# Performance work log

Measured on AMD Instinct MI355X. Metric: run time of the kernel, lower is better.

## Reference

```python
import jax, jax.numpy as jnp
import numpy as np

D_MODEL = 1024
NUM_HEADS = 16
OUT_SHAPE = (64,)            # ControlGate `shape`; d_head = prod(OUT_SHAPE)
BANK_SIZE = 16
TOP_K = 2
BATCH, SEQ = 8, 4096
D_OUT = NUM_HEADS * int(np.prod(OUT_SHAPE))  # 1024


def setup_inputs() -> dict:
    key = jax.random.key(0)
    k1, k2, k3, k4 = jax.random.split(key, 4)
    tensor = jax.random.normal(k1, (BATCH, SEQ, D_MODEL), dtype=jnp.float32)
    sel_idx = jax.random.randint(k2, (BATCH, TOP_K), 0, BANK_SIZE)
    sel_probs = jax.random.uniform(k3, (BATCH, TOP_K), dtype=jnp.float32)
    sel_probs = sel_probs / jnp.sum(sel_probs, axis=-1, keepdims=True)
    W = jax.random.normal(k4, (BANK_SIZE, D_MODEL, D_OUT), dtype=jnp.float32) * 0.02
    b = jnp.zeros((BANK_SIZE, D_OUT), dtype=jnp.float32)
    return {"tensor": tensor, "sel_idx": sel_idx, "sel_probs": sel_probs, "W": W, "b": b}


def reference(tensor, sel_idx, sel_probs, W, b):
    # --- VirtualMakeHeads: bank-selected (virtual) linear projection ---
    # Superimpose the selected weight banks per batch element.
    W_sel = W[sel_idx]                    # (B, K, d_model, d_out)  irregular gather
    b_sel = b[sel_idx]                    # (B, K, d_out)
    W_eff = jnp.einsum('bk,bkio->bio', sel_probs, W_sel)   # (B, d_model, d_out)
    b_eff = jnp.einsum('bk,bko->bo', sel_probs, b_sel)     # (B, d_out)
    logits = jnp.einsum('bsi,bio->bso', tensor, W_eff) + b_eff[:, None, :]
    # reshape to heads: (B, S, num_heads, d_head)
    logits = logits.reshape(*logits.shape[:-1], NUM_HEADS, -1)
    # --- ControlGate: unflatten last dim into OUT_SHAPE ---
    logits = logits.reshape(*logits.shape[:-1], *OUT_SHAPE)
    # DropoutLogits with p=0.0 (eval) is identity.
    # activation == 'sigmoid'
    return jax.nn.sigmoid(logits)
```

## Files before the change

### kernel.cpp

```cpp
#include <hip/hip_runtime.h>
#include <hip/hip_bf16.h>

#define B_  8
#define S_  4096
#define DM  1024
#define DO  1024

typedef __attribute__((ext_vector_type(4))) float f32x4;
typedef __attribute__((ext_vector_type(8))) short bf16x8;

__device__ inline unsigned int pkbf(float a, float b) {
    __hip_bfloat162 h = __float22bfloat162_rn(float2{a, b});
    union { __hip_bfloat162 h2; unsigned int u; } cv;
    cv.h2 = h;
    return cv.u;
}

__global__ __launch_bounds__(256) void prep_wpack(
    const float* __restrict__ W, const int* __restrict__ sel_idx,
    const float* __restrict__ sel_probs, unsigned short* __restrict__ wpack)
{
    const int kt = blockIdx.x, nb = blockIdx.y, b = blockIdx.z;
    const int i0 = sel_idx[b*2+0], i1 = sel_idx[b*2+1];
    const float p0 = sel_probs[b*2+0], p1 = sel_probs[b*2+1];
    const int col = threadIdx.x;
    const int half = col >> 7, colh = col & 127;

    const float* w0 = W + (size_t)i0 * DM * DO + (size_t)(kt * 64) * DO + nb * 256 + col;
    const float* w1 = W + (size_t)i1 * DM * DO + (size_t)(kt * 64) * DO + nb * 256 + col;

    char* dst = (char*)wpack + ((((size_t)b * 4 + nb) * 16 + kt) << 15)
              + half * 16384 + colh * 128;

    #pragma unroll
    for (int g = 0; g < 8; ++g) {
        float v[8];
        #pragma unroll
        for (int j = 0; j < 8; ++j)
            v[j] = p0 * w0[(size_t)(g * 8 + j) * DO] + p1 * w1[(size_t)(g * 8 + j) * DO];
        uint4 u;
        u.x = pkbf(v[0], v[1]); u.y = pkbf(v[2], v[3]);
        u.z = pkbf(v[4], v[5]); u.w = pkbf(v[6], v[7]);
        *reinterpret_cast<uint4*>(dst + ((g * 16) ^ ((colh & 7) << 4))) = u;
    }
}

__global__ __launch_bounds__(256) void prep_beff(
    const float* __restrict__ bias, const int* __restrict__ sel_idx,
    const float* __restrict__ sel_probs, float* __restrict__ beff)
{
    const int b = blockIdx.x;
    const int i0 = sel_idx[b*2+0], i1 = sel_idx[b*2+1];
    const float p0 = sel_probs[b*2+0], p1 = sel_probs[b*2+1];
    for (int o = threadIdx.x; o < DO; o += blockDim.x)
        beff[(size_t)b * DO + o] = p0 * bias[(size_t)i0 * DO + o]
                                 + p1 * bias[(size_t)i1 * DO + o];
}

__global__ __launch_bounds__(512, 1) void gemm8(
    const float* __restrict__ X, const unsigned short* __restrict__ wpack,
    const float* __restrict__ beff, float* __restrict__ out)
{
    extern __shared__ char lds[];

    const int id = blockIdx.x;
    const int swz = (id & 7) * 64 + (id >> 3);
    const int b  = swz >> 6;
    const int bm = (swz & 63) >> 2;
    const int nb = swz & 3;

    const int t = threadIdx.x;
    const int wave = t >> 6, lane = t & 63;
    const int wm = wave >> 2, wn = wave & 3;
    const int fr = lane & 15, fq = lane >> 4;

    const int s_row = t >> 3;
    const int s_g   = t & 7;
    const float* xbase = X + ((size_t)(b * S_ + bm * 256 + s_row)) * DM + s_g * 8;
    const char* wtile0 = (const char*)(wpack + (((size_t)b * 4 + nb) * 16) * 16384);

    const int swz0 = (fq * 16) ^ ((fr & 7) << 4);
    const int swz1 = (64 + fq * 16) ^ ((fr & 7) << 4);
    const int aTb = wm * 16384 + fr * 128;
    const int bTb = (wn >> 1) * 16384 + ((wn & 1) * 64 + fr) * 128;

    f32x4 acc[8][4] = {};
    float4 ax[8];

#define LOAD_X(KT)                                                            \
    _Pragma("unroll")                                                         \
    for (int p = 0; p < 4; ++p) {                                             \
        ax[p*2]   = *reinterpret_cast<const float4*>(xbase + (size_t)p*64*DM + (KT)*64);     \
        ax[p*2+1] = *reinterpret_cast<const float4*>(xbase + (size_t)p*64*DM + (KT)*64 + 4); \
    }

#define STAGE_B(KT, BOFF)                                                     \
    {                                                                         \
        const char* gB = wtile0 + (size_t)(KT) * 32768;                       \
        _Pragma("unroll")                                                     \
        for (int i = 0; i < 4; ++i)                                           \
            __builtin_amdgcn_global_load_lds(                                 \
                (const __attribute__((address_space(1))) void*)(gB + wave*4096 + i*1024 + lane*16), \
                (__attribute__((address_space(3))) void*)(lds + (BOFF) + wave*4096 + i*1024),       \
                16, 0, 0);                                                    \
    }

#define WRITE_A()                                                             \
    _Pragma("unroll")                                                         \
    for (int p = 0; p < 4; ++p) {                                             \
        const int row = p * 64 + s_row;                                       \
        const int half = row >> 7, rowh = row & 127;                          \
        uint4 u;                                                              \
        u.x = pkbf(ax[p*2].x, ax[p*2].y);     u.y = pkbf(ax[p*2].z, ax[p*2].w);     \
        u.z = pkbf(ax[p*2+1].x, ax[p*2+1].y); u.w = pkbf(ax[p*2+1].z, ax[p*2+1].w); \
        *reinterpret_cast<uint4*>(lds + half*16384 + rowh*128                 \
                                  + ((s_g*16) ^ ((rowh & 7) << 4))) = u;      \
    }

    LOAD_X(0);
    __builtin_amdgcn_sched_barrier(0);
    STAGE_B(0, 32768);
    STAGE_B(1, 65536);
    __builtin_amdgcn_sched_barrier(0);
    WRITE_A();
    asm volatile("s_waitcnt vmcnt(4) lgkmcnt(0)" ::: "memory");
    __builtin_amdgcn_s_barrier();

    int br = 32768, bmid = 65536, bw = 98304;

    for (int kt = 0; kt < 16; ++kt) {
        if (kt < 15) { LOAD_X(kt + 1); }
        __builtin_amdgcn_sched_barrier(0);
        if (kt < 14) { STAGE_B(kt + 2, bw); }
        __builtin_amdgcn_sched_barrier(0);

        const char* Bb = lds + br;
        bf16x8 bks[4], af[4];

#define PHASE(MFBASE, SK, RELOAD_B)                                           \
        {                                                                     \
            if (RELOAD_B) {                                                   \
                _Pragma("unroll")                                             \
                for (int nf = 0; nf < 4; ++nf)                                \
                    bks[nf] = *reinterpret_cast<const bf16x8*>(Bb + bTb + nf*2048 + (SK)); \
            }                                                                 \
            _Pragma("unroll")                                                 \
            for (int m = 0; m < 4; ++m)                                       \
                af[m] = *reinterpret_cast<const bf16x8*>(lds + aTb + ((MFBASE)+m)*2048 + (SK)); \
            __builtin_amdgcn_s_barrier();                                     \
            __builtin_amdgcn_s_setprio(1);                                    \
            _Pragma("unroll")                                                 \
            for (int m = 0; m < 4; ++m) {                                     \
                _Pragma("unroll")                                             \
                for (int nf = 0; nf < 4; ++nf)                                \
                    acc[(MFBASE)+m][nf] = __builtin_amdgcn_mfma_f32_16x16x32_bf16( \
                        af[m], bks[nf], acc[(MFBASE)+m][nf], 0, 0, 0);        \
            }                                                                 \
            __builtin_amdgcn_s_setprio(0);                                    \
            __builtin_amdgcn_s_barrier();                                     \
        }

        PHASE(0, swz0, 1)
        PHASE(4, swz0, 0)
        PHASE(0, swz1, 1)
        PHASE(4, swz1, 0)
#undef PHASE

        if (kt < 15) {
            WRITE_A();
            asm volatile("s_waitcnt lgkmcnt(0)" ::: "memory");
            __builtin_amdgcn_s_barrier();
        }
        const int tmp = br; br = bmid; bmid = bw; bw = tmp;
    }

    const float* be = beff + (size_t)b * DO + nb * 256 + wn * 64;
    float bv[4];
    #pragma unroll
    for (int nf = 0; nf < 4; ++nf) bv[nf] = be[nf * 16 + fr];

    float* ob = out + ((size_t)(b * S_ + bm * 256 + wm * 128)) * DO + nb * 256 + wn * 64;
    #pragma unroll
    for (int mf = 0; mf < 8; ++mf) {
        #pragma unroll
        for (int nf = 0; nf < 4; ++nf) {
            const int col = nf * 16 + fr;
            #pragma unroll
            for (int r = 0; r < 4; ++r) {
                const int row = mf * 16 + fq * 4 + r;
                const float xv = acc[mf][nf][r] + bv[nf];
                ob[(size_t)row * DO + col] = 1.0f / (1.0f + __expf(-xv));
            }
        }
    }
#undef LOAD_X
#undef STAGE_B
#undef WRITE_A
}

extern "C" void kernel_launch(void* const* d_in, const int* in_sizes, int n_in,
                              void* d_out, int out_size, void* d_ws, size_t ws_size,
                              hipStream_t stream) {
    const float* tensor    = (const float*)d_in[0];
    const int*   sel_idx   = (const int*)d_in[1];
    const float* sel_probs = (const float*)d_in[2];
    const float* W         = (const float*)d_in[3];
    const float* bias      = (const float*)d_in[4];
    float* out = (float*)d_out;

    unsigned short* wpack = (unsigned short*)d_ws;
    float* beff = (float*)((char*)d_ws + (size_t)B_ * 4 * 16 * 32768);

    hipFuncSetAttribute((const void*)gemm8,
                        hipFuncAttributeMaxDynamicSharedMemorySize, 131072);

    hipLaunchKernelGGL(prep_wpack, dim3(16, 4, 8), dim3(256), 0, stream,
                       W, sel_idx, sel_probs, wpack);
    hipLaunchKernelGGL(prep_beff, dim3(8), dim3(256), 0, stream,
                       bias, sel_idx, sel_probs, beff);
    hipLaunchKernelGGL(gemm8, dim3(512), dim3(512), 131072, stream,
                       tensor, wpack, beff, out);
}
```

Measured before the change: 143.0 us.

## Double-buffer A and B in LDS with register-prefetched fragments, one barrier per k-tile

Restructures the GEMM main loop. A gets a double-buffered LDS slot, and B drops from triple to double buffering. Fragments for the next MFMA block are read from LDS into registers while the current MFMA block runs, so the four per-phase barrier pairs are replaced by a single barrier per k-tile. This aims to cut synchronisation stalls and overlap LDS reads with MFMA work. In exchange it raises register pressure from the extra fragment arrays, and the full vmcnt(0) wait each iteration may expose global load latency.

```diff
diff --git a/kernel.cpp b/kernel.cpp
--- a/kernel.cpp
+++ b/kernel.cpp
@@ -105,7 +105,7 @@
                 16, 0, 0);                                                    \
     }
 
-#define WRITE_A()                                                             \
+#define WRITE_A(AOFF)                                                         \
     _Pragma("unroll")                                                         \
     for (int p = 0; p < 4; ++p) {                                             \
         const int row = p * 64 + s_row;                                       \
@@ -113,66 +113,84 @@
         uint4 u;                                                              \
         u.x = pkbf(ax[p*2].x, ax[p*2].y);     u.y = pkbf(ax[p*2].z, ax[p*2].w);     \
         u.z = pkbf(ax[p*2+1].x, ax[p*2+1].y); u.w = pkbf(ax[p*2+1].z, ax[p*2+1].w); \
-        *reinterpret_cast<uint4*>(lds + half*16384 + rowh*128                 \
+        *reinterpret_cast<uint4*>(lds + (AOFF) + half*16384 + rowh*128        \
                                   + ((s_g*16) ^ ((rowh & 7) << 4))) = u;      \
     }
+
+#define READ_A4(DST, AOFF, MFBASE, SWZ)                                       \
+    _Pragma("unroll")                                                         \
+    for (int m = 0; m < 4; ++m)                                               \
+        DST[m] = *reinterpret_cast<const bf16x8*>(lds + (AOFF) + aTb + ((MFBASE)+m)*2048 + (SWZ));
+
+#define READ_B4(DST, BOFF, SWZ)                                               \
+    _Pragma("unroll")                                                         \
+    for (int nf = 0; nf < 4; ++nf)                                            \
+        DST[nf] = *reinterpret_cast<const bf16x8*>(lds + (BOFF) + bTb + nf*2048 + (SWZ));
+
+#define MFMA16(MFBASE, AF, BK)                                                \
+    __builtin_amdgcn_s_setprio(1);                                            \
+    _Pragma("unroll")                                                         \
+    for (int m = 0; m < 4; ++m) {                                             \
+        _Pragma("unroll")                                                     \
+        for (int nf = 0; nf < 4; ++nf)                                        \
+            acc[(MFBASE)+m][nf] = __builtin_amdgcn_mfma_f32_16x16x32_bf16(    \
+                AF[m], BK[nf], acc[(MFBASE)+m][nf], 0, 0, 0);                 \
+    }                                                                         \
+    __builtin_amdgcn_s_setprio(0);
 
     LOAD_X(0);
     __builtin_amdgcn_sched_barrier(0);
-    STAGE_B(0, 32768);
-    STAGE_B(1, 65536);
+    STAGE_B(0, 65536);
     __builtin_amdgcn_sched_barrier(0);
-    WRITE_A();
-    asm volatile("s_waitcnt vmcnt(4) lgkmcnt(0)" ::: "memory");
+    WRITE_A(0);
+    asm volatile("s_waitcnt vmcnt(0) lgkmcnt(0)" ::: "memory");
     __builtin_amdgcn_s_barrier();
-
-    int br = 32768, bmid = 65536, bw = 98304;
-
-    for (int kt = 0; kt < 16; ++kt) {
-        if (kt < 15) { LOAD_X(kt + 1); }
+    __builtin_amdgcn_sched_barrier(0);
+
+    bf16x8 afA[4], afB[4], afC[4], afD[4], bksA[4], bksB[4];
+    int a_cur = 0, a_nxt = 32768, b_cur = 65536, b_nxt = 98304;
+
+    READ_A4(afA, a_cur, 0, swz0);
+    READ_B4(bksA, b_cur, swz0);
+
+    #pragma unroll 1
+    for (int kt = 0; kt < 15; ++kt) {
+        LOAD_X(kt + 1);
         __builtin_amdgcn_sched_barrier(0);
-        if (kt < 14) { STAGE_B(kt + 2, bw); }
+        STAGE_B(kt + 1, b_nxt);
         __builtin_amdgcn_sched_barrier(0);
 
-        const char* Bb = lds + br;
-        bf16x8 bks[4], af[4];
-
-#define PHASE(MFBASE, SK, RELOAD_B)                                           \
-        {                                                                     \
-            if (RELOAD_B) {                                                   \
-                _Pragma("unroll")                                             \
-                for (int nf = 0; nf < 4; ++nf)                                \
-                    bks[nf] = *reinterpret_cast<const bf16x8*>(Bb + bTb + nf*2048 + (SK)); \
-            }                                                                 \
-            _Pragma("unroll")                                                 \
-            for (int m = 0; m < 4; ++m)                                       \
-                af[m] = *reinterpret_cast<const bf16x8*>(lds + aTb + ((MFBASE)+m)*2048 + (SK)); \
-            __builtin_amdgcn_s_barrier();                                     \
-            __builtin_amdgcn_s_setprio(1);                                    \
-            _Pragma("unroll")                                                 \
-            for (int m = 0; m < 4; ++m) {                                     \
-                _Pragma("unroll")                                             \
-                for (int nf = 0; nf < 4; ++nf)                                \
-                    acc[(MFBASE)+m][nf] = __builtin_amdgcn_mfma_f32_16x16x32_bf16( \
-                        af[m], bks[nf], acc[(MFBASE)+m][nf], 0, 0, 0);        \
-            }                                                                 \
-            __builtin_amdgcn_s_setprio(0);                                    \
-            __builtin_amdgcn_s_barrier();                                     \
-        }
-
-        PHASE(0, swz0, 1)
-        PHASE(4, swz0, 0)
-        PHASE(0, swz1, 1)
-        PHASE(4, swz1, 0)
-#undef PHASE
-
-        if (kt < 15) {
-            WRITE_A();
-            asm volatile("s_waitcnt lgkmcnt(0)" ::: "memory");
-            __builtin_amdgcn_s_barrier();
-        }
-        const int tmp = br; br = bmid; bmid = bw; bw = tmp;
-    }
+        READ_A4(afB, a_cur, 4, swz0);
+        MFMA16(0, afA, bksA);
+
+        READ_A4(afC, a_cur, 0, swz1);
+        READ_B4(bksB, b_cur, swz1);
+        MFMA16(4, afB, bksA);
+
+        READ_A4(afD, a_cur, 4, swz1);
+        MFMA16(0, afC, bksB);
+
+        WRITE_A(a_nxt);
+        asm volatile("s_waitcnt vmcnt(0) lgkmcnt(0)" ::: "memory");
+        __builtin_amdgcn_s_barrier();
+        __builtin_amdgcn_sched_barrier(0);
+
+        READ_A4(afA, a_nxt, 0, swz0);
+        READ_B4(bksA, b_nxt, swz0);
+        MFMA16(4, afD, bksB);
+
+        int tmp = a_cur; a_cur = a_nxt; a_nxt = tmp;
+        tmp = b_cur; b_cur = b_nxt; b_nxt = tmp;
+    }
+
+    READ_A4(afB, a_cur, 4, swz0);
+    MFMA16(0, afA, bksA);
+    READ_A4(afC, a_cur, 0, swz1);
+    READ_B4(bksB, b_cur, swz1);
+    MFMA16(4, afB, bksA);
+    READ_A4(afD, a_cur, 4, swz1);
+    MFMA16(0, afC, bksB);
+    MFMA16(4, afD, bksB);
 
     const float* be = beff + (size_t)b * DO + nb * 256 + wn * 64;
     float bv[4];
@@ -196,6 +214,9 @@
 #undef LOAD_X
 #undef STAGE_B
 #undef WRITE_A
+#undef READ_A4
+#undef READ_B4
+#undef MFMA16
 }
 
 extern "C" void kernel_launch(void* const* d_in, const int* in_sizes, int n_in,
```

Result: no change. 143.5 us (+0.4%).
